# Performance work log

Hardware: AMD Instinct MI355X
Metric: run time of the kernel (lower is better)

Reference implementation:

```python
import math
import jax, jax.numpy as jnp
import numpy as np

B, H, S, D = 2, 16, 2048, 128

def setup_inputs() -> dict:
    key = jax.random.key(0)
    kq, kk, kv, km = jax.random.split(key, 4)
    q = jax.random.normal(kq, (B, H, S, D), dtype=jnp.float32)
    k = jax.random.normal(kk, (B, H, S, D), dtype=jnp.float32)
    v = jax.random.normal(kv, (B, H, S, D), dtype=jnp.float32)
    mask = jax.random.randint(km, (B, 1, S, S), 0, 2, dtype=jnp.int32)
    return {"q": q, "k": k, "v": v, "mask": mask}

def reference(q, k, v, mask):
    d_tensor = k.shape[-1]
    # score = q @ k^T / sqrt(d)
    score = jnp.einsum("bhqd,bhkd->bhqk", q, k) / jnp.sqrt(jnp.float32(d_tensor))
    # faithful to torch: masked positions are set to 1e-09 (not -inf) before softmax
    score = jnp.where(mask == 0, jnp.float32(1e-09), score)
    score = jax.nn.softmax(score, axis=-1)
    out = jnp.einsum("bhqk,bhkd->bhqd", score, v)
    return (out, score)
```

## Files before the change

### kernel.cpp

```cpp
#include <hip/hip_runtime.h>


#define S_LEN 2048
#define DH 128
#define NT 32
#define SCALE 0.088388347648318447f

typedef short short8_t __attribute__((ext_vector_type(8)));
typedef float f32x4_t __attribute__((ext_vector_type(4)));
typedef unsigned short u16x4_t __attribute__((ext_vector_type(4)));
typedef unsigned int u32x4_t __attribute__((ext_vector_type(4)));

__device__ __forceinline__ unsigned short f2bf(float x) {
  union { float f; unsigned u; } c; c.f = x;
  return (unsigned short)((c.u + 0x7FFFu + ((c.u >> 16) & 1u)) >> 16);
}
__device__ __forceinline__ float bf2f(unsigned short b) {
  union { float f; unsigned u; } c; c.u = ((unsigned)b) << 16;
  return c.f;
}
__device__ __forceinline__ void gll16(const void* g, void* l) {
  __builtin_amdgcn_global_load_lds(
      (const __attribute__((address_space(1))) unsigned int*)g,
      (__attribute__((address_space(3))) unsigned int*)l, 16, 0, 0);
}
__device__ __forceinline__ unsigned pk2(unsigned short a, unsigned short b) {
  return (unsigned)a | ((unsigned)b << 16);
}


__global__ void pack_mask_k(const int* __restrict__ M, unsigned long long* __restrict__ bm) {
  int g = (blockIdx.x * 256 + threadIdx.x) >> 6;
  int lane = threadIdx.x & 63;
#pragma unroll
  for (int i = 0; i < 16; ++i) {
    int w = g * 16 + i;
    int v = M[(size_t)w * 64 + lane];
    unsigned long long bits = __ballot(v != 0);
    if (lane == 0) bm[w] = bits;
  }
}

__global__ void conv_k_k(const float* __restrict__ K, unsigned short* __restrict__ kws) {
  int c = blockIdx.x * 256 + threadIdx.x;
  int tile = c >> 10;
  int p = (c & 1023) * 16;
  int r = p >> 8, X = p & 255;
  int d0 = (X ^ ((r & 7) << 4)) >> 1;
  int bh = tile >> 5, k = (tile & 31) * 64 + r;
  const float* src = K + ((size_t)bh * S_LEN + k) * DH + d0;
  f32x4_t a = *(const f32x4_t*)src;
  f32x4_t b = *(const f32x4_t*)(src + 4);
  u32x4_t o = { pk2(f2bf(a[0]), f2bf(a[1])), pk2(f2bf(a[2]), f2bf(a[3])),
                pk2(f2bf(b[0]), f2bf(b[1])), pk2(f2bf(b[2]), f2bf(b[3])) };
  *(u32x4_t*)((char*)kws + (size_t)tile * 16384 + p) = o;
}

__global__ void conv_v_k(const float* __restrict__ V, unsigned short* __restrict__ vws) {
  __shared__ unsigned short vt[64 * 132];
  int tile = blockIdx.x, bh = tile >> 5, kt = tile & 31;
  int tid = threadIdx.x;
  const float* src = V + ((size_t)bh * S_LEN + kt * 64) * DH;
#pragma unroll
  for (int pass = 0; pass < 8; ++pass) {
    int idx = pass * 256 + tid;
    int row = idx >> 5, d0 = (idx & 31) * 4;
    f32x4_t a = *(const f32x4_t*)(src + (size_t)row * DH + d0);
    u16x4_t w = { f2bf(a[0]), f2bf(a[1]), f2bf(a[2]), f2bf(a[3]) };
    *(u16x4_t*)&vt[row * 132 + d0] = w;
  }
  __syncthreads();
#pragma unroll
  for (int c4 = 0; c4 < 4; ++c4) {
    int chunk = c4 * 256 + tid;
    int p = chunk * 16;
    int d = p >> 7, X = p & 127;
    int kv0 = (X ^ ((d & 7) << 4)) >> 1;
    unsigned short e[8];
#pragma unroll
    for (int i = 0; i < 8; ++i) e[i] = vt[(kv0 + i) * 132 + d];
    u32x4_t o = { pk2(e[0], e[1]), pk2(e[2], e[3]), pk2(e[4], e[5]), pk2(e[6], e[7]) };
    *(u32x4_t*)((char*)vws + (size_t)tile * 16384 + p) = o;
  }
}


__global__ __launch_bounds__(512, 4)
void sdpa_fused(const float* __restrict__ Q,
                const unsigned short* __restrict__ kws,
                const unsigned short* __restrict__ vws,
                const unsigned long long* __restrict__ bm,
                float* __restrict__ Out, float* __restrict__ Sc) {
  extern __shared__ char smem[];
  char* kst = smem;
  unsigned short* pbB = (unsigned short*)(smem + 65536);
  float* lpart = (float*)(smem + 65536 + 9216);
  float* rinv  = lpart + 128;

  const int tid = threadIdx.x;
  const int lane = tid & 63, wid = tid >> 6;
  const int qh = wid >> 2, kq = wid & 3;
  const int lg = lane >> 4, ln = lane & 15;

  const int wg = blockIdx.x;
  const int j = wg >> 3;
  const int bh = (wg & 7) * 4 + (j >> 6);
  const int qt = j & 63;
  const int b = bh >> 4;
  const int q0 = qt * 32;

  short8_t qf[4];
  {
    const float* qrow = Q + ((size_t)bh * S_LEN + q0 + qh * 16 + ln) * DH;
#pragma unroll
    for (int kk = 0; kk < 4; ++kk) {
      f32x4_t a = *(const f32x4_t*)(qrow + kk * 32 + lg * 8);
      f32x4_t c = *(const f32x4_t*)(qrow + kk * 32 + lg * 8 + 4);
      short8_t f;
#pragma unroll
      for (int jj = 0; jj < 4; ++jj) { f[jj] = (short)f2bf(a[jj]); f[4 + jj] = (short)f2bf(c[jj]); }
      qf[kk] = f;
    }
  }

  const char* ktiles = (const char*)kws + (size_t)bh * NT * 16384;
  const char* vtiles = (const char*)vws + (size_t)bh * NT * 16384;
  const int stoff = wid * 1024 + lane * 16;
  const int ldoff = wid * 1024;

  const unsigned long long* bmr = bm + ((size_t)b * S_LEN + q0 + qh * 16 + lg * 4) * NT;
  const int krow = kq * 16 + ln;
  const int arow = qh * 16 + ln;
  const int bitp = kq * 16 + ln;
  const int pbase = (qh * 16 + lg * 4) * 72 + kq * 16 + ln;

  float psum[4] = {0.f, 0.f, 0.f, 0.f};

  gll16(ktiles + stoff,                 kst + ldoff);
  gll16(ktiles + stoff + 8192,          kst + ldoff + 8192);
  gll16(ktiles + 16384 + stoff,         kst + 16384 + ldoff);
  gll16(ktiles + 16384 + stoff + 8192,  kst + 16384 + ldoff + 8192);
  gll16(ktiles + 32768 + stoff,         kst + 32768 + ldoff);
  gll16(ktiles + 32768 + stoff + 8192,  kst + 32768 + ldoff + 8192);
  __builtin_amdgcn_sched_barrier(0);
  unsigned long long ma0 = bmr[0], ma1 = bmr[NT], ma2 = bmr[2 * NT], ma3 = bmr[3 * NT];
  asm volatile("s_waitcnt vmcnt(8) lgkmcnt(0)\n\ts_barrier" ::: "memory");
  __builtin_amdgcn_sched_barrier(0);

#pragma unroll
  for (int kt = 0; kt < NT; ++kt) {
    if (kt < NT - 3) {
      const char* gk = ktiles + (size_t)(kt + 3) * 16384 + stoff;
      char* dst = kst + ((kt + 3) & 3) * 16384 + ldoff;
      gll16(gk, dst);
      gll16(gk + 8192, dst + 8192);
    }
    __builtin_amdgcn_sched_barrier(0);
    unsigned long long c0 = ma0, c1 = ma1, c2 = ma2, c3 = ma3;
    if (kt < NT - 1) {
      ma0 = bmr[kt + 1]; ma1 = bmr[NT + kt + 1];
      ma2 = bmr[2 * NT + kt + 1]; ma3 = bmr[3 * NT + kt + 1];
    }
    const char* kbc = kst + (kt & 3) * 16384;
    f32x4_t acc = {0.f, 0.f, 0.f, 0.f};
#pragma unroll
    for (int kk = 0; kk < 4; ++kk) {
      short8_t bfr = *(const short8_t*)(kbc + krow * 256 + ((kk * 64 + lg * 16) ^ ((krow & 7) << 4)));
      acc = __builtin_amdgcn_mfma_f32_16x16x32_bf16(qf[kk], bfr, acc, 0, 0, 0);
    }
    psum[0] += ((c0 >> bitp) & 1) ? __expf(acc[0] * SCALE) : 1.0f;
    psum[1] += ((c1 >> bitp) & 1) ? __expf(acc[1] * SCALE) : 1.0f;
    psum[2] += ((c2 >> bitp) & 1) ? __expf(acc[2] * SCALE) : 1.0f;
    psum[3] += ((c3 >> bitp) & 1) ? __expf(acc[3] * SCALE) : 1.0f;
    if (kt == 0) {
      asm volatile("s_waitcnt vmcnt(12) lgkmcnt(0)\n\ts_barrier" ::: "memory");
    } else if (kt <= 28) {
      asm volatile("s_waitcnt vmcnt(16) lgkmcnt(0)\n\ts_barrier" ::: "memory");
    } else if (kt == 29) {
      asm volatile("s_waitcnt vmcnt(14) lgkmcnt(0)\n\ts_barrier" ::: "memory");
    } else if (kt == 30) {
      asm volatile("s_waitcnt vmcnt(12) lgkmcnt(0)\n\ts_barrier" ::: "memory");
    }
    __builtin_amdgcn_sched_barrier(0);
  }

#pragma unroll
  for (int off = 1; off < 16; off <<= 1) {
#pragma unroll
    for (int jj = 0; jj < 4; ++jj) psum[jj] += __shfl_xor(psum[jj], off, 64);
  }
  if (ln == 0) {
#pragma unroll
    for (int jj = 0; jj < 4; ++jj) lpart[kq * 32 + qh * 16 + lg * 4 + jj] = psum[jj];
  }
  __syncthreads();
  if (tid < 32)
    rinv[tid] = 1.0f / (lpart[tid] + lpart[32 + tid] + lpart[64 + tid] + lpart[96 + tid]);
  __syncthreads();

  char* kbb = kst;
  char* vbb = kst + 32768;
  const int sr = tid >> 4, sc4 = (tid & 15) * 4;
  const float ri_s = rinv[sr];
  float* scp = Sc + ((size_t)bh * S_LEN + q0 + sr) * S_LEN + sc4;

  gll16(ktiles + stoff,        kbb + ldoff);
  gll16(ktiles + stoff + 8192, kbb + ldoff + 8192);
  gll16(vtiles + stoff,        vbb + ldoff);
  gll16(vtiles + stoff + 8192, vbb + ldoff + 8192);
  __builtin_amdgcn_sched_barrier(0);
  ma0 = bmr[0]; ma1 = bmr[NT]; ma2 = bmr[2 * NT]; ma3 = bmr[3 * NT];
  asm volatile("s_waitcnt vmcnt(4) lgkmcnt(0)\n\ts_barrier" ::: "memory");
  __builtin_amdgcn_sched_barrier(0);

  f32x4_t oacc0 = {0.f, 0.f, 0.f, 0.f}, oacc1 = {0.f, 0.f, 0.f, 0.f};

#pragma unroll 2
  for (int kt = 0; kt < NT; ++kt) {
    const int cur = kt & 1, nxt = cur ^ 1;
    if (kt < NT - 1) {
      const char* gk = ktiles + (size_t)(kt + 1) * 16384 + stoff;
      const char* gv = vtiles + (size_t)(kt + 1) * 16384 + stoff;
      gll16(gk,        kbb + nxt * 16384 + ldoff);
      gll16(gk + 8192, kbb + nxt * 16384 + ldoff + 8192);
      gll16(gv,        vbb + nxt * 16384 + ldoff);
      gll16(gv + 8192, vbb + nxt * 16384 + ldoff + 8192);
    }
    __builtin_amdgcn_sched_barrier(0);
    unsigned long long c0 = ma0, c1 = ma1, c2 = ma2, c3 = ma3;
    if (kt < NT - 1) {
      ma0 = bmr[kt + 1]; ma1 = bmr[NT + kt + 1];
      ma2 = bmr[2 * NT + kt + 1]; ma3 = bmr[3 * NT + kt + 1];
    }
    const char* kbc = kbb + cur * 16384;
    f32x4_t acc = {0.f, 0.f, 0.f, 0.f};
#pragma unroll
    for (int kk = 0; kk < 4; ++kk) {
      short8_t bfr = *(const short8_t*)(kbc + krow * 256 + ((kk * 64 + lg * 16) ^ ((krow & 7) << 4)));
      acc = __builtin_amdgcn_mfma_f32_16x16x32_bf16(qf[kk], bfr, acc, 0, 0, 0);
    }
    float p0 = ((c0 >> bitp) & 1) ? __expf(acc[0] * SCALE) : 1.0f;
    float p1 = ((c1 >> bitp) & 1) ? __expf(acc[1] * SCALE) : 1.0f;
    float p2 = ((c2 >> bitp) & 1) ? __expf(acc[2] * SCALE) : 1.0f;
    float p3 = ((c3 >> bitp) & 1) ? __expf(acc[3] * SCALE) : 1.0f;
    unsigned short* pbc = pbB + cur * 2304;
    pbc[pbase]       = f2bf(p0);
    pbc[pbase + 72]  = f2bf(p1);
    pbc[pbase + 144] = f2bf(p2);
    pbc[pbase + 216] = f2bf(p3);
    asm volatile("s_waitcnt lgkmcnt(0)\n\ts_barrier" ::: "memory");
    __builtin_amdgcn_sched_barrier(0);
    {
      u16x4_t w = *(const u16x4_t*)&pbc[sr * 72 + sc4];
      f32x4_t o = { bf2f(w[0]) * ri_s, bf2f(w[1]) * ri_s, bf2f(w[2]) * ri_s, bf2f(w[3]) * ri_s };
      __builtin_nontemporal_store(o, (f32x4_t*)(scp + kt * 64));
    }
    const char* vbc = vbb + cur * 16384;
    short8_t af0 = *(const short8_t*)((const char*)pbc + arow * 144 + lg * 16);
    short8_t af1 = *(const short8_t*)((const char*)pbc + arow * 144 + 64 + lg * 16);
    {
      const int vr0 = kq * 32 + ln;
      short8_t bv0 = *(const short8_t*)(vbc + vr0 * 128 + ((lg * 16) ^ ((vr0 & 7) << 4)));
      short8_t bv1 = *(const short8_t*)(vbc + vr0 * 128 + ((64 + lg * 16) ^ ((vr0 & 7) << 4)));
      oacc0 = __builtin_amdgcn_mfma_f32_16x16x32_bf16(af0, bv0, oacc0, 0, 0, 0);
      oacc0 = __builtin_amdgcn_mfma_f32_16x16x32_bf16(af1, bv1, oacc0, 0, 0, 0);
    }
    {
      const int vr1 = kq * 32 + 16 + ln;
      short8_t bv0 = *(const short8_t*)(vbc + vr1 * 128 + ((lg * 16) ^ ((vr1 & 7) << 4)));
      short8_t bv1 = *(const short8_t*)(vbc + vr1 * 128 + ((64 + lg * 16) ^ ((vr1 & 7) << 4)));
      oacc1 = __builtin_amdgcn_mfma_f32_16x16x32_bf16(af0, bv0, oacc1, 0, 0, 0);
      oacc1 = __builtin_amdgcn_mfma_f32_16x16x32_bf16(af1, bv1, oacc1, 0, 0, 0);
    }
    asm volatile("s_waitcnt vmcnt(5) lgkmcnt(0)\n\ts_barrier" ::: "memory");
    __builtin_amdgcn_sched_barrier(0);
  }

#pragma unroll
  for (int jj = 0; jj < 4; ++jj) {
    int row = qh * 16 + lg * 4 + jj;
    float ri = rinv[row];
    size_t o = ((size_t)bh * S_LEN + q0 + row) * DH + kq * 32 + ln;
    __builtin_nontemporal_store(oacc0[jj] * ri, &Out[o]);
    __builtin_nontemporal_store(oacc1[jj] * ri, &Out[o + 16]);
  }
}


#define PT_STRIDE 2056
#define KLDS_STRIDE 136
#define VT_STRIDE 72

__global__ __launch_bounds__(512, 1)
void sdpa_kernel_v1(const float* __restrict__ Q, const float* __restrict__ K,
                    const float* __restrict__ V, const int* __restrict__ M,
                    float* __restrict__ Out, float* __restrict__ Sc) {
  extern __shared__ char smem[];
  unsigned short* pt  = (unsigned short*)smem;
  unsigned short* kvb = (unsigned short*)(smem + 131584);
  float* lpart = (float*)(smem + 131584 + 18432);
  float* rinv  = lpart + 128;

  const int tid  = threadIdx.x;
  const int lane = tid & 63;
  const int wid  = tid >> 6;
  const int qh = wid >> 2, kq = wid & 3;
  const int lg = lane >> 4, ln = lane & 15;

  const int bid = blockIdx.x;
  const int qt = bid & 63, bh = bid >> 6, b = bh >> 4;
  const int q0 = qt * 32;

  const float* Qb = Q + ((size_t)bh * S_LEN + q0) * DH;
  const float* Kb = K + (size_t)bh * S_LEN * DH;
  const float* Vb = V + (size_t)bh * S_LEN * DH;
  const int*   Mb = M + ((size_t)b * S_LEN + q0) * (size_t)S_LEN;

  short8_t qf[4];
  {
    const float* qrow = Qb + (qh * 16 + ln) * DH;
#pragma unroll
    for (int kk = 0; kk < 4; ++kk) {
      f32x4_t a = *(const f32x4_t*)(qrow + kk * 32 + lg * 8);
      f32x4_t c = *(const f32x4_t*)(qrow + kk * 32 + lg * 8 + 4);
      short8_t f;
#pragma unroll
      for (int jj = 0; jj < 4; ++jj) { f[jj] = (short)f2bf(a[jj]); f[4 + jj] = (short)f2bf(c[jj]); }
      qf[kk] = f;
    }
  }

  float psum[4] = {0.f, 0.f, 0.f, 0.f};

  for (int kt = 0; kt < 32; ++kt) {
    const int k0 = kt * 64;
    __syncthreads();
#pragma unroll
    for (int p = 0; p < 4; ++p) {
      int idx = (p << 11) | (tid << 2);
      int r = idx >> 7, d0 = idx & 127;
      f32x4_t val = *(const f32x4_t*)(Kb + (size_t)(k0 + r) * DH + d0);
      u16x4_t w = { f2bf(val[0]), f2bf(val[1]), f2bf(val[2]), f2bf(val[3]) };
      *(u16x4_t*)&kvb[r * KLDS_STRIDE + d0] = w;
    }
    __syncthreads();

    const int kcol = k0 + kq * 16 + ln;
    int mv[4];
#pragma unroll
    for (int jj = 0; jj < 4; ++jj)
      mv[jj] = Mb[(size_t)(qh * 16 + lg * 4 + jj) * S_LEN + kcol];

    f32x4_t acc = {0.f, 0.f, 0.f, 0.f};
#pragma unroll
    for (int kk = 0; kk < 4; ++kk) {
      short8_t bf = *(short8_t*)&kvb[(kq * 16 + ln) * KLDS_STRIDE + kk * 32 + lg * 8];
      acc = __builtin_amdgcn_mfma_f32_16x16x32_bf16(qf[kk], bf, acc, 0, 0, 0);
    }
#pragma unroll
    for (int jj = 0; jj < 4; ++jj) {
      float p = mv[jj] ? __expf(acc[jj] * SCALE) : 1.0f;
      psum[jj] += p;
      pt[(qh * 16 + lg * 4 + jj) * PT_STRIDE + kcol] = f2bf(p);
    }
  }

#pragma unroll
  for (int off = 1; off < 16; off <<= 1) {
#pragma unroll
    for (int jj = 0; jj < 4; ++jj) psum[jj] += __shfl_xor(psum[jj], off, 64);
  }
  if (ln == 0) {
#pragma unroll
    for (int jj = 0; jj < 4; ++jj) lpart[kq * 32 + qh * 16 + lg * 4 + jj] = psum[jj];
  }
  __syncthreads();
  if (tid < 32)
    rinv[tid] = 1.0f / (lpart[tid] + lpart[32 + tid] + lpart[64 + tid] + lpart[96 + tid]);
  __syncthreads();

  {
    float* srow = Sc + ((size_t)bh * S_LEN + q0) * (size_t)S_LEN;
#pragma unroll 4
    for (int r = 0; r < 32; ++r) {
      float ri = rinv[r];
      u16x4_t w = *(u16x4_t*)&pt[r * PT_STRIDE + tid * 4];
      f32x4_t o = { bf2f(w[0]) * ri, bf2f(w[1]) * ri, bf2f(w[2]) * ri, bf2f(w[3]) * ri };
      *(f32x4_t*)(srow + (size_t)r * S_LEN + tid * 4) = o;
    }
  }

  const int dq = kq;
  f32x4_t oacc0 = {0.f,0.f,0.f,0.f}, oacc1 = {0.f,0.f,0.f,0.f};
  const int dcol = tid & 127, qq = tid >> 7;
  for (int vt = 0; vt < 32; ++vt) {
    const int k0 = vt * 64;
    __syncthreads();
#pragma unroll
    for (int p = 0; p < 4; ++p) {
      int krb = p * 16 + qq * 4;
      const float* vp = Vb + (size_t)(k0 + krb) * DH + dcol;
      float v0 = vp[0], v1 = vp[DH], v2 = vp[2 * DH], v3 = vp[3 * DH];
      u16x4_t w = { f2bf(v0), f2bf(v1), f2bf(v2), f2bf(v3) };
      *(u16x4_t*)&kvb[dcol * VT_STRIDE + krb] = w;
    }
    __syncthreads();
#pragma unroll
    for (int ks = 0; ks < 2; ++ks) {
      short8_t af = *(short8_t*)&pt[(qh * 16 + ln) * PT_STRIDE + k0 + ks * 32 + lg * 8];
#pragma unroll
      for (int nb = 0; nb < 2; ++nb) {
        short8_t bf = *(short8_t*)&kvb[(dq * 32 + nb * 16 + ln) * VT_STRIDE + ks * 32 + lg * 8];
        if (nb == 0) oacc0 = __builtin_amdgcn_mfma_f32_16x16x32_bf16(af, bf, oacc0, 0, 0, 0);
        else         oacc1 = __builtin_amdgcn_mfma_f32_16x16x32_bf16(af, bf, oacc1, 0, 0, 0);
      }
    }
  }
#pragma unroll
  for (int jj = 0; jj < 4; ++jj) {
    int row = qh * 16 + lg * 4 + jj;
    float ri = rinv[row];
    size_t o = ((size_t)bh * S_LEN + q0 + row) * DH + dq * 32 + ln;
    Out[o]      = oacc0[jj] * ri;
    Out[o + 16] = oacc1[jj] * ri;
  }
}


extern "C" void kernel_launch(void* const* d_in, const int* in_sizes, int n_in,
                              void* d_out, int out_size, void* d_ws, size_t ws_size,
                              hipStream_t stream) {
  const float* q = (const float*)d_in[0];
  const float* k = (const float*)d_in[1];
  const float* v = (const float*)d_in[2];
  const int*   m = (const int*)d_in[3];
  float* out = (float*)d_out;
  float* sc  = out + (size_t)2 * 16 * S_LEN * DH;

  const size_t BM_BYTES = 1u << 20;
  const size_t KW_BYTES = (size_t)32 * 32 * 16384;
  const size_t NEED = BM_BYTES + 2 * KW_BYTES;

  if (ws_size >= NEED) {
    unsigned long long* bm = (unsigned long long*)d_ws;
    unsigned short* kws = (unsigned short*)((char*)d_ws + BM_BYTES);
    unsigned short* vws = (unsigned short*)((char*)d_ws + BM_BYTES + KW_BYTES);

    pack_mask_k<<<dim3(2048), dim3(256), 0, stream>>>(m, bm);
    conv_k_k<<<dim3(4096), dim3(256), 0, stream>>>(k, kws);
    conv_v_k<<<dim3(1024), dim3(256), 0, stream>>>(v, vws);

    const int smem = 65536 + 9216 + 512 + 128;
    hipFuncSetAttribute((const void*)sdpa_fused,
                        hipFuncAttributeMaxDynamicSharedMemorySize, smem);
    sdpa_fused<<<dim3(2048), dim3(512), smem, stream>>>(q, kws, vws, bm, out, sc);
  } else {
    const int smem = 131584 + 18432 + 512 + 128;
    hipFuncSetAttribute((const void*)sdpa_kernel_v1,
                        hipFuncAttributeMaxDynamicSharedMemorySize, smem);
    sdpa_kernel_v1<<<dim3(2048), dim3(512), smem, stream>>>(q, k, v, m, out, sc);
  }
}
```

Baseline: 307.4 us.

## Triple-buffer probability tiles, batch score stores per two tiles, and raise MFMA priority

The P staging buffer becomes triple-buffered, so score-matrix stores can be issued every other tile, with each thread writing 8 floats covering two consecutive key tiles. This halves the number of store instructions issued and relaxes the trailing barrier wait counts. It also wraps the MFMA sections in s_setprio(1) so matrix work is favoured over the other waves' memory traffic. The cost is more LDS per block (9216 to 13824 bytes for the buffer), which may lower occupancy, plus more complex vmcnt bookkeeping.

```diff
diff --git a/kernel.cpp b/kernel.cpp
--- a/kernel.cpp
+++ b/kernel.cpp
@@ -94,7 +94,7 @@
   extern __shared__ char smem[];
   char* kst = smem;
   unsigned short* pbB = (unsigned short*)(smem + 65536);
-  float* lpart = (float*)(smem + 65536 + 9216);
+  float* lpart = (float*)(smem + 65536 + 13824);
   float* rinv  = lpart + 128;
 
   const int tid = threadIdx.x;
@@ -163,11 +163,13 @@
     }
     const char* kbc = kst + (kt & 3) * 16384;
     f32x4_t acc = {0.f, 0.f, 0.f, 0.f};
+    __builtin_amdgcn_s_setprio(1);
 #pragma unroll
     for (int kk = 0; kk < 4; ++kk) {
       short8_t bfr = *(const short8_t*)(kbc + krow * 256 + ((kk * 64 + lg * 16) ^ ((krow & 7) << 4)));
       acc = __builtin_amdgcn_mfma_f32_16x16x32_bf16(qf[kk], bfr, acc, 0, 0, 0);
     }
+    __builtin_amdgcn_s_setprio(0);
     psum[0] += ((c0 >> bitp) & 1) ? __expf(acc[0] * SCALE) : 1.0f;
     psum[1] += ((c1 >> bitp) & 1) ? __expf(acc[1] * SCALE) : 1.0f;
     psum[2] += ((c2 >> bitp) & 1) ? __expf(acc[2] * SCALE) : 1.0f;
@@ -200,9 +202,11 @@
 
   char* kbb = kst;
   char* vbb = kst + 32768;
-  const int sr = tid >> 4, sc4 = (tid & 15) * 4;
+  const int sr = tid >> 4;
+  const int shalf = (tid >> 3) & 1;
+  const int sc8 = (tid & 7) * 8;
   const float ri_s = rinv[sr];
-  float* scp = Sc + ((size_t)bh * S_LEN + q0 + sr) * S_LEN + sc4;
+  float* scp = Sc + ((size_t)bh * S_LEN + q0 + sr) * S_LEN + (tid & 15) * 8;
 
   gll16(ktiles + stoff,        kbb + ldoff);
   gll16(ktiles + stoff + 8192, kbb + ldoff + 8192);
@@ -234,30 +238,39 @@
     }
     const char* kbc = kbb + cur * 16384;
     f32x4_t acc = {0.f, 0.f, 0.f, 0.f};
+    __builtin_amdgcn_s_setprio(1);
 #pragma unroll
     for (int kk = 0; kk < 4; ++kk) {
       short8_t bfr = *(const short8_t*)(kbc + krow * 256 + ((kk * 64 + lg * 16) ^ ((krow & 7) << 4)));
       acc = __builtin_amdgcn_mfma_f32_16x16x32_bf16(qf[kk], bfr, acc, 0, 0, 0);
     }
+    __builtin_amdgcn_s_setprio(0);
     float p0 = ((c0 >> bitp) & 1) ? __expf(acc[0] * SCALE) : 1.0f;
     float p1 = ((c1 >> bitp) & 1) ? __expf(acc[1] * SCALE) : 1.0f;
     float p2 = ((c2 >> bitp) & 1) ? __expf(acc[2] * SCALE) : 1.0f;
     float p3 = ((c3 >> bitp) & 1) ? __expf(acc[3] * SCALE) : 1.0f;
-    unsigned short* pbc = pbB + cur * 2304;
+    unsigned short* pbc = pbB + (kt % 3) * 2304;
     pbc[pbase]       = f2bf(p0);
     pbc[pbase + 72]  = f2bf(p1);
     pbc[pbase + 144] = f2bf(p2);
     pbc[pbase + 216] = f2bf(p3);
     asm volatile("s_waitcnt lgkmcnt(0)\n\ts_barrier" ::: "memory");
     __builtin_amdgcn_sched_barrier(0);
-    {
-      u16x4_t w = *(const u16x4_t*)&pbc[sr * 72 + sc4];
-      f32x4_t o = { bf2f(w[0]) * ri_s, bf2f(w[1]) * ri_s, bf2f(w[2]) * ri_s, bf2f(w[3]) * ri_s };
-      __builtin_nontemporal_store(o, (f32x4_t*)(scp + kt * 64));
+    if (kt & 1) {
+      const unsigned short* pbs = pbB + ((kt - 1 + shalf) % 3) * 2304;
+      short8_t pw = *(const short8_t*)&pbs[sr * 72 + sc8];
+      f32x4_t s0 = { bf2f((unsigned short)pw[0]) * ri_s, bf2f((unsigned short)pw[1]) * ri_s,
+                     bf2f((unsigned short)pw[2]) * ri_s, bf2f((unsigned short)pw[3]) * ri_s };
+      f32x4_t s1 = { bf2f((unsigned short)pw[4]) * ri_s, bf2f((unsigned short)pw[5]) * ri_s,
+                     bf2f((unsigned short)pw[6]) * ri_s, bf2f((unsigned short)pw[7]) * ri_s };
+      float* dst = scp + (kt - 1) * 64;
+      __builtin_nontemporal_store(s0, (f32x4_t*)dst);
+      __builtin_nontemporal_store(s1, (f32x4_t*)(dst + 4));
     }
     const char* vbc = vbb + cur * 16384;
     short8_t af0 = *(const short8_t*)((const char*)pbc + arow * 144 + lg * 16);
     short8_t af1 = *(const short8_t*)((const char*)pbc + arow * 144 + 64 + lg * 16);
+    __builtin_amdgcn_s_setprio(1);
     {
       const int vr0 = kq * 32 + ln;
       short8_t bv0 = *(const short8_t*)(vbc + vr0 * 128 + ((lg * 16) ^ ((vr0 & 7) << 4)));
@@ -272,7 +285,14 @@
       oacc1 = __builtin_amdgcn_mfma_f32_16x16x32_bf16(af0, bv0, oacc1, 0, 0, 0);
       oacc1 = __builtin_amdgcn_mfma_f32_16x16x32_bf16(af1, bv1, oacc1, 0, 0, 0);
     }
-    asm volatile("s_waitcnt vmcnt(5) lgkmcnt(0)\n\ts_barrier" ::: "memory");
+    __builtin_amdgcn_s_setprio(0);
+    if (kt < NT - 1) {
+      if (kt & 1) {
+        asm volatile("s_waitcnt vmcnt(6) lgkmcnt(0)\n\ts_barrier" ::: "memory");
+      } else {
+        asm volatile("s_waitcnt vmcnt(4) lgkmcnt(0)\n\ts_barrier" ::: "memory");
+      }
+    }
     __builtin_amdgcn_sched_barrier(0);
   }
 
@@ -298,8 +318,8 @@
   extern __shared__ char smem[];
   unsigned short* pt  = (unsigned short*)smem;
   unsigned short* kvb = (unsigned short*)(smem + 131584);
-  float* lpart = (float*)(smem + 131584 + 18432);
-  float* rinv  = lpart + 128;
+  float* lpart2 = (float*)(smem + 131584 + 18432);
+  float* rinv2  = lpart2 + 128;
 
   const int tid  = threadIdx.x;
   const int lane = tid & 63;
@@ -372,18 +392,18 @@
   }
   if (ln == 0) {
 #pragma unroll
-    for (int jj = 0; jj < 4; ++jj) lpart[kq * 32 + qh * 16 + lg * 4 + jj] = psum[jj];
+    for (int jj = 0; jj < 4; ++jj) lpart2[kq * 32 + qh * 16 + lg * 4 + jj] = psum[jj];
   }
   __syncthreads();
   if (tid < 32)
-    rinv[tid] = 1.0f / (lpart[tid] + lpart[32 + tid] + lpart[64 + tid] + lpart[96 + tid]);
+    rinv2[tid] = 1.0f / (lpart2[tid] + lpart2[32 + tid] + lpart2[64 + tid] + lpart2[96 + tid]);
   __syncthreads();
 
   {
     float* srow = Sc + ((size_t)bh * S_LEN + q0) * (size_t)S_LEN;
 #pragma unroll 4
     for (int r = 0; r < 32; ++r) {
-      float ri = rinv[r];
+      float ri = rinv2[r];
       u16x4_t w = *(u16x4_t*)&pt[r * PT_STRIDE + tid * 4];
       f32x4_t o = { bf2f(w[0]) * ri, bf2f(w[1]) * ri, bf2f(w[2]) * ri, bf2f(w[3]) * ri };
       *(f32x4_t*)(srow + (size_t)r * S_LEN + tid * 4) = o;
@@ -419,7 +439,7 @@
 #pragma unroll
   for (int jj = 0; jj < 4; ++jj) {
     int row = qh * 16 + lg * 4 + jj;
-    float ri = rinv[row];
+    float ri = rinv2[row];
     size_t o = ((size_t)bh * S_LEN + q0 + row) * DH + dq * 32 + ln;
     Out[o]      = oacc0[jj] * ri;
     Out[o + 16] = oacc1[jj] * ri;
@@ -450,7 +470,7 @@
     conv_k_k<<<dim3(4096), dim3(256), 0, stream>>>(k, kws);
     conv_v_k<<<dim3(1024), dim3(256), 0, stream>>>(v, vws);
 
-    const int smem = 65536 + 9216 + 512 + 128;
+    const int smem = 65536 + 13824 + 512 + 128;
     hipFuncSetAttribute((const void*)sdpa_fused,
                         hipFuncAttributeMaxDynamicSharedMemorySize, smem);
     sdpa_fused<<<dim3(2048), dim3(512), smem, stream>>>(q, kws, vws, bm, out, sc);
```

Measured after the change: 335.8 us. 1.09x slower.
